# Kernel tuning notes

Measured on AMD Instinct MI355X. Metric: run time of the kernel, lower is better.

## Reference

```python
import jax, jax.numpy as jnp
import numpy as np

B, KOBJ, NS, NK = 32, 100, 16, 8
EMB, FEAT, HID, OUT, COMB = 1024, 2052, 1024, 3000, 512


def _pseudo_coord(bb_centre):
    # bb_centre (B,K,2) -> polar pseudo coords (B,K,K,2) = (rho, theta)
    d = bb_centre[:, :, None, :] - bb_centre[:, None, :, :]
    rho = jnp.sqrt(d[..., 0] ** 2 + d[..., 1] ** 2)
    theta = jnp.arctan2(d[..., 0], d[..., 1])
    return jnp.stack([rho, theta], axis=-1)


def _gauss_weights(pseudo, mr, mt, pr, pt):
    # pseudo (B,K,NS,2); kernel params (NK,) -> weights (B,K,NS,NK)
    rho = pseudo[..., 0:1]
    theta = pseudo[..., 1:2]
    w_rho = jnp.exp(-0.5 * (rho - mr) ** 2 / (1e-14 + pr ** 2))
    fa = jnp.abs(theta - mt)
    sa = jnp.abs(2.0 * jnp.pi - fa)
    w_th = jnp.exp(-0.5 * jnp.minimum(fa, sa) ** 2 / (1e-14 + pt ** 2))
    w = w_rho * w_th
    w = jnp.where(jnp.isnan(w), 0.0, w)
    return w / jnp.sum(w, axis=-1, keepdims=True)  # normalise over kernels


def _graph_conv(feats, pseudo, conv_w, mr, mt, pr, pt):
    # feats (B,K,NS,F), conv_w (NK,F,out_k) -> (B,K,NK*out_k)
    w = _gauss_weights(pseudo, mr, mt, pr, pt)          # (B,K,NS,NK)
    agg = jnp.einsum('bksm,bksf->bkmf', w, feats)       # per-kernel neighbour sum
    out = jnp.einsum('bkmf,mfo->bkmo', agg, conv_w)     # per-kernel linear
    return out.reshape(out.shape[0], out.shape[1], -1)  # kernel-major concat


def _neighbourhood(feats, pseudo, adj, weight):
    # topk over adjacency rows; softmax over topk values (== the per-row loop softmax)
    top_v, top_i = jax.lax.top_k(adj, NS)               # (B,K,NS)
    a = jax.nn.softmax(top_v, axis=-1)
    nb_f = jax.vmap(lambda f, i: f[i])(feats, top_i)    # (B,K,NS,F)
    nb_p = jnp.take_along_axis(pseudo, top_i[..., None], axis=2)  # (B,K,NS,2)
    if weight:
        nb_f = a[..., None] * nb_f
    return nb_f, nb_p


def _forward(question, image, K, W_lproj, b_lproj, W_e1, b_e1, W_e2, b_e2,
             conv_w1, mean_rho1, mean_theta1, prec_rho1, prec_theta1,
             conv_w2, mean_rho2, mean_theta2, prec_rho2, prec_theta2,
             W_o1, b_o1, W_o2, b_o2):
    bb = image[:, :, -4:]
    bb_size = bb[:, :, 2:] - bb[:, :, :2]
    bb_centre = bb[:, :, :2] + 0.5 * bb_size
    pseudo = _pseudo_coord(bb_centre)                   # (B,K,K,2)

    qenc = question @ W_lproj + b_lproj                 # (B,HID)
    qrep = jnp.broadcast_to(qenc[:, None, :], (image.shape[0], K, qenc.shape[-1]))
    cat = jnp.concatenate([image, qrep], axis=-1)       # (B,K,FEAT+HID)

    # GraphLearner: two relu linears then gram matrix
    h = jax.nn.relu(cat @ W_e1 + b_e1)
    h = jax.nn.relu(h @ W_e2 + b_e2)                    # (B,K,COMB)
    adj = jnp.einsum('bkc,blc->bkl', h, h)              # (B,K,K)

    nb_f, nb_p = _neighbourhood(image, pseudo, adj, weight=True)
    g1 = jax.nn.relu(_graph_conv(nb_f, nb_p, conv_w1, mean_rho1, mean_theta1, prec_rho1, prec_theta1))
    nb_f2, nb_p2 = _neighbourhood(g1, pseudo, adj, weight=False)
    g2 = jax.nn.relu(_graph_conv(nb_f2, nb_p2, conv_w2, mean_rho2, mean_theta2, prec_rho2, prec_theta2))
    g2 = jnp.max(g2, axis=1)                            # (B,HID)

    hh = jax.nn.relu(qenc) * g2
    h1 = jax.nn.relu(hh @ W_o1 + b_o1)
    logits = h1 @ W_o2 + b_o2
    return logits, adj


def setup_inputs() -> dict:
    key = jax.random.key(0)
    ks = jax.random.split(key, 17)
    s = jnp.float32(0.02)
    f32 = jnp.float32
    inp = {
        'question': jax.random.normal(ks[0], (B, EMB), f32),
        'image': jax.random.uniform(ks[1], (B, KOBJ, FEAT), f32),
        'K': KOBJ,
        'W_lproj': jax.random.normal(ks[2], (EMB, HID), f32) * s,
        'b_lproj': jnp.zeros((HID,), f32),
        'W_e1': jax.random.normal(ks[3], (FEAT + HID, COMB), f32) * s,
        'b_e1': jnp.zeros((COMB,), f32),
        'W_e2': jax.random.normal(ks[4], (COMB, COMB), f32) * s,
        'b_e2': jnp.zeros((COMB,), f32),
        'conv_w1': jax.random.normal(ks[5], (NK, FEAT, 2 * HID // NK), f32) * s,
        'mean_rho1': jax.random.uniform(ks[6], (NK,), f32),
        'mean_theta1': jax.random.uniform(ks[7], (NK,), f32, -np.pi, np.pi),
        'prec_rho1': jax.random.uniform(ks[8], (NK,), f32),
        'prec_theta1': jax.random.uniform(ks[9], (NK,), f32),
        'conv_w2': jax.random.normal(ks[10], (NK, 2 * HID, HID // NK), f32) * s,
        'mean_rho2': jax.random.uniform(ks[11], (NK,), f32),
        'mean_theta2': jax.random.uniform(ks[12], (NK,), f32, -np.pi, np.pi),
        'prec_rho2': jax.random.uniform(ks[13], (NK,), f32),
        'prec_theta2': jax.random.uniform(ks[14], (NK,), f32),
        'W_o1': jax.random.normal(ks[15], (HID, OUT), f32) * s,
        'b_o1': jnp.zeros((OUT,), f32),
        'W_o2': jax.random.normal(ks[16], (OUT, OUT), f32) * s,
        'b_o2': jnp.zeros((OUT,), f32),
    }
    return inp


def reference(question, image, K, W_lproj, b_lproj, W_e1, b_e1, W_e2, b_e2,
              conv_w1, mean_rho1, mean_theta1, prec_rho1, prec_theta1,
              conv_w2, mean_rho2, mean_theta2, prec_rho2, prec_theta2,
              W_o1, b_o1, W_o2, b_o2):
    return _forward(question, image, K, W_lproj, b_lproj, W_e1, b_e1, W_e2, b_e2,
                    conv_w1, mean_rho1, mean_theta1, prec_rho1, prec_theta1,
                    conv_w2, mean_rho2, mean_theta2, prec_rho2, prec_theta2,
                    W_o1, b_o1, W_o2, b_o2)
```

## Files before the change

### kernel.cpp

```cpp
#include <hip/hip_runtime.h>
#include <math.h>
#include <stdint.h>

#define B_    32
#define KOBJ  100
#define NS_   16
#define NK_   8
#define EMB_  1024
#define FEAT_ 2052
#define HID_  1024
#define OUT_  3000
#define COMB_ 512

#define KP1   2112
#define KP2   2048
#define NO_P  3072
#define KO2   3008

typedef __attribute__((ext_vector_type(8))) short s16x8;
typedef __attribute__((ext_vector_type(4))) float f32x4;

__device__ inline short f2bf(float f) {
  uint32_t u = __builtin_bit_cast(uint32_t, f);
  u = (u + 0x7fff + ((u >> 16) & 1)) >> 16;
  return (short)u;
}
__device__ inline float bf2f(short s) {
  uint32_t u = ((uint32_t)(uint16_t)s) << 16;
  return __builtin_bit_cast(float, u);
}
__device__ inline void gload_lds16(const void* g, void* l) {
  __builtin_amdgcn_global_load_lds(
      (const __attribute__((address_space(1))) void*)g,
      (__attribute__((address_space(3))) void*)l, 16, 0, 0);
}
__device__ inline int xcd_remap(int fid, int nwg) {
  int q = nwg >> 3, r = nwg & 7;
  int x = fid & 7, l = fid >> 3;
  return (x < r ? x * (q + 1) : r * (q + 1) + (x - r) * q) + l;
}

#define IMG_CHUNKS (B_ * KOBJ * (KP1 / 8))
#define IMG_BLKS   ((IMG_CHUNKS + 255) / 256)
#define Q_CHUNKS   (B_ * (EMB_ / 8))
#define Q_BLKS     ((Q_CHUNKS + 255) / 256)
#define C_BLKS     ((B_ * KOBJ + 255) / 256)

__device__ inline void cvt8_split(const float* __restrict__ in, short* __restrict__ oh,
                                  short* __restrict__ ol, int K, int Kp, int idx) {
  int row = idx / (Kp / 8), c8 = (idx % (Kp / 8)) * 8;
  float f[8];
  if (c8 + 8 <= K) {
    const float* src = in + (size_t)row * K + c8;
    float4 a = *(const float4*)src;
    float4 b = *(const float4*)(src + 4);
    f[0] = a.x; f[1] = a.y; f[2] = a.z; f[3] = a.w;
    f[4] = b.x; f[5] = b.y; f[6] = b.z; f[7] = b.w;
  } else {
#pragma unroll
    for (int i = 0; i < 8; ++i) {
      int k = c8 + i;
      f[i] = (k < K) ? in[(size_t)row * K + k] : 0.f;
    }
  }
  s16x8 vh, vl;
#pragma unroll
  for (int i = 0; i < 8; ++i) {
    short h = f2bf(f[i]);
    vh[i] = h;
    vl[i] = f2bf(f[i] - bf2f(h));
  }
  *(s16x8*)(oh + (size_t)row * Kp + c8) = vh;
  *(s16x8*)(ol + (size_t)row * Kp + c8) = vl;
}

struct TD {
  const float* in; short* oh; short* ol;
  int K, N, Kp, OPM, nkt, split, conv, cum;
};
struct TDs { TD d[8]; };

__global__ __launch_bounds__(256) void prep_all(
    TDs ds, int tcum,
    const float* __restrict__ image, const float* __restrict__ question,
    short* __restrict__ imgb, short* __restrict__ imgl,
    short* __restrict__ qh, short* __restrict__ ql, float* __restrict__ cent) {
  int bid = blockIdx.x, t = threadIdx.x;
  if (bid >= tcum) {
    int bb = bid - tcum;
    if (bb < IMG_BLKS) {
      int idx = bb * 256 + t;
      if (idx < IMG_CHUNKS) cvt8_split(image, imgb, imgl, FEAT_, KP1, idx);
    } else if (bb < IMG_BLKS + Q_BLKS) {
      int idx = (bb - IMG_BLKS) * 256 + t;
      if (idx < Q_CHUNKS) cvt8_split(question, qh, ql, EMB_, EMB_, idx);
    } else {
      int i = (bb - IMG_BLKS - Q_BLKS) * 256 + t;
      if (i < B_ * KOBJ) {
        const float* bbx = image + (size_t)i * FEAT_ + (FEAT_ - 4);
        cent[i * 2 + 0] = 0.5f * (bbx[0] + bbx[2]);
        cent[i * 2 + 1] = 0.5f * (bbx[1] + bbx[3]);
      }
    }
    return;
  }
  __shared__ float s[64][65];
  int i = 0;
  while (i < 7 && bid >= ds.d[i].cum) ++i;
  const TD& d = ds.d[i];
  int local = bid - (i ? ds.d[i - 1].cum : 0);
  int k0 = (local % d.nkt) * 64, n0 = (local / d.nkt) * 64;
  int rr = t >> 4, c4 = (t & 15) * 4;
  bool fullN = d.conv || (n0 + 64 <= d.N);
#pragma unroll
  for (int p = 0; p < 4; ++p) {
    int row = p * 16 + rr;
    int kg = k0 + row;
    float v0 = 0.f, v1 = 0.f, v2 = 0.f, v3 = 0.f;
    if (kg < d.K) {
      const float* src = d.conv
          ? d.in + ((size_t)(n0 / d.OPM) * d.K + kg) * d.OPM + (n0 % d.OPM) + c4
          : d.in + (size_t)kg * d.N + n0 + c4;
      if (fullN) {
        float4 v = *(const float4*)src;
        v0 = v.x; v1 = v.y; v2 = v.z; v3 = v.w;
      } else {
        int nb = n0 + c4;
        if (nb + 0 < d.N) v0 = src[0];
        if (nb + 1 < d.N) v1 = src[1];
        if (nb + 2 < d.N) v2 = src[2];
        if (nb + 3 < d.N) v3 = src[3];
      }
    }
    s[row][c4 + 0] = v0; s[row][c4 + 1] = v1;
    s[row][c4 + 2] = v2; s[row][c4 + 3] = v3;
  }
  __syncthreads();
  int nl = t >> 2, kc = (t & 3) << 4;
#pragma unroll
  for (int half = 0; half < 2; ++half) {
    s16x8 vh, vl;
#pragma unroll
    for (int j = 0; j < 8; ++j) {
      float f = s[kc + half * 8 + j][nl];
      short h = f2bf(f);
      vh[j] = h;
      vl[j] = f2bf(f - bf2f(h));
    }
    size_t o = (size_t)(n0 + nl) * d.Kp + k0 + kc + half * 8;
    *(s16x8*)(d.oh + o) = vh;
    if (d.split) *(s16x8*)(d.ol + o) = vl;
  }
}

template <int BM, int BN, int WR, int WC, bool SPLIT, bool RELU, bool BIAS, int OMODE,
          bool SPLITK, bool PB16>
__device__ __forceinline__ void gemm_body(
    char* smem, int bx, int by, int bz,
    const short* __restrict__ Ah, const short* __restrict__ Al,
    const short* __restrict__ Bh, const short* __restrict__ Bl,
    const float* __restrict__ bias,
    float* __restrict__ Cf, short* __restrict__ Ch, short* __restrict__ Cl,
    float* __restrict__ part, short* __restrict__ partb, int KS,
    int M, int N, int Kp, int ldc, int Nw) {
  constexpr int NWV = WR * WC;
  constexpr int WM = BM / WR, WN = BN / WC;
  constexpr int FM = WM / 16, FN = WN / 16;
  constexpr int ACH = BM / 8, BCH = BN / 8;
  constexpr int NCH = (ACH + BCH) * (SPLIT ? 2 : 1);
  char* AshC = smem;
  char* BshC = smem + BM * 128;
  char* AslC = smem + (BM + BN) * 128;
  char* BslC = smem + (2 * BM + BN) * 128;
  int tid = threadIdx.x, wave = tid >> 6, lane = tid & 63;
  int wr = wave / WC, wc = wave % WC;
  int r16 = lane & 15, kq = lane >> 4;
  int m0 = by * BM, n0 = bx * BN;
  int kb = SPLITK ? bz * KS : 0;
  int ke = SPLITK ? (kb + KS < Kp ? kb + KS : Kp) : Kp;
  f32x4 acc[FM][FN] = {};

  for (int k0 = kb; k0 < ke; k0 += 64) {
    __syncthreads();
    for (int c = wave; c < NCH; c += NWV) {
      int cc = c;
      const short* g;
      char* l;
      bool isA;
      if (cc < ACH) { isA = true; g = Ah; l = AshC; }
      else if (SPLIT && cc < 2 * ACH) { cc -= ACH; isA = true; g = Al; l = AslC; }
      else {
        cc -= SPLIT ? 2 * ACH : ACH;
        if (cc < BCH) { isA = false; g = Bh; l = BshC; }
        else { cc -= BCH; isA = false; g = Bl; l = BslC; }
      }
      int Lb = cc * 1024 + lane * 16;
      int row = Lb >> 7;
      int off = (Lb & 127) ^ ((row & 7) << 4);
      const short* gsrc = g + (size_t)((isA ? m0 : n0) + row) * Kp + k0 + (off >> 1);
      gload_lds16(gsrc, l + cc * 1024);
    }
    __syncthreads();
#pragma unroll
    for (int kk = 0; kk < 2; ++kk) {
      int woff = kk * 64 + kq * 16;
      s16x8 ah[FM], al[FM], bh[FN], bl[FN];
#pragma unroll
      for (int f = 0; f < FM; ++f) {
        int row = wr * WM + f * 16 + r16;
        int o = woff ^ ((row & 7) << 4);
        ah[f] = *(const s16x8*)(AshC + row * 128 + o);
        if (SPLIT) al[f] = *(const s16x8*)(AslC + row * 128 + o);
      }
#pragma unroll
      for (int gg = 0; gg < FN; ++gg) {
        int row = wc * WN + gg * 16 + r16;
        int o = woff ^ ((row & 7) << 4);
        bh[gg] = *(const s16x8*)(BshC + row * 128 + o);
        if (SPLIT) bl[gg] = *(const s16x8*)(BslC + row * 128 + o);
      }
#pragma unroll
      for (int f = 0; f < FM; ++f)
#pragma unroll
        for (int gg = 0; gg < FN; ++gg) {
          acc[f][gg] = __builtin_amdgcn_mfma_f32_16x16x32_bf16(ah[f], bh[gg], acc[f][gg], 0, 0, 0);
          if (SPLIT) {
            acc[f][gg] = __builtin_amdgcn_mfma_f32_16x16x32_bf16(ah[f], bl[gg], acc[f][gg], 0, 0, 0);
            acc[f][gg] = __builtin_amdgcn_mfma_f32_16x16x32_bf16(al[f], bh[gg], acc[f][gg], 0, 0, 0);
          }
        }
    }
  }
#pragma unroll
  for (int f = 0; f < FM; ++f)
#pragma unroll
    for (int gg = 0; gg < FN; ++gg)
#pragma unroll
      for (int r = 0; r < 4; ++r) {
        int m = m0 + wr * WM + f * 16 + (lane >> 4) * 4 + r;
        int n = n0 + wc * WN + gg * 16 + r16;
        if (m >= M || n >= Nw) continue;
        float v = (n < N) ? acc[f][gg][r] : 0.f;
        size_t idx = (size_t)m * ldc + n;
        if (SPLITK) {
          size_t pidx = (size_t)bz * M * ldc + idx;
          if (PB16) partb[pidx] = f2bf(v);
          else      part[pidx] = v;
        } else {
          if (BIAS && n < N) v += bias[n];
          if (RELU) v = fmaxf(v, 0.f);
          if (OMODE == 0) Cf[idx] = v;
          else if (OMODE == 1) {
            short h = f2bf(v);
            Ch[idx] = h;
            Cl[idx] = f2bf(v - bf2f(h));
          } else if (OMODE == 2) {
            Ch[idx] = f2bf(v);
          } else {
            Cf[idx] = v;
            short h = f2bf(v);
            Ch[idx] = h;
            Cl[idx] = f2bf(v - bf2f(h));
          }
        }
      }
}

template <int BM, int BN, int WR, int WC, bool SPLIT, bool RELU, bool BIAS, int OMODE,
          bool SPLITK, bool PB16>
__global__ __launch_bounds__(WR * WC * 64) void gemm_mx(
    const short* __restrict__ Ah, const short* __restrict__ Al,
    const short* __restrict__ Bh, const short* __restrict__ Bl,
    const float* __restrict__ bias,
    float* __restrict__ Cf, short* __restrict__ Ch, short* __restrict__ Cl,
    float* __restrict__ part, short* __restrict__ partb, int KS,
    int M, int N, int Kp, int ldc, int Nw) {
  __shared__ char smem_s[(BM + BN) * 128 * (SPLIT ? 2 : 1)];
  int gx = gridDim.x, gy = gridDim.y, gz = gridDim.z;
  int fid = (blockIdx.z * gy + blockIdx.y) * gx + blockIdx.x;
  int wg = xcd_remap(fid, gx * gy * gz);
  int bx = wg % gx, byz = wg / gx;
  int by = byz % gy, bz = byz / gy;
  gemm_body<BM, BN, WR, WC, SPLIT, RELU, BIAS, OMODE, SPLITK, PB16>(
      smem_s, bx, by, bz, Ah, Al, Bh, Bl, bias, Cf, Ch, Cl, part, partb, KS,
      M, N, Kp, ldc, Nw);
}

#define E1B 800
#define P1B 400
__global__ __launch_bounds__(512) void fused_e1_proj1(
    const short* __restrict__ imgb, const short* __restrict__ imgl,
    const short* __restrict__ we1ah, const short* __restrict__ we1al,
    float* __restrict__ partE,
    const short* __restrict__ cw1t, short* __restrict__ proj1b) {
  extern __shared__ char smem[];
  int fid = blockIdx.x;
  if (fid < E1B) {
    int wg = xcd_remap(fid, E1B);
    int gx = COMB_ / 64;
    int bx = wg % gx, t = wg / gx;
    int by = t % (B_ * KOBJ / 128), bz = t / (B_ * KOBJ / 128);
    gemm_body<128, 64, 4, 2, true, false, false, 0, true, false>(
        smem, bx, by, bz, imgb, imgl, we1ah, we1al, nullptr,
        nullptr, nullptr, nullptr, partE, nullptr, 576,
        B_ * KOBJ, COMB_, KP1, COMB_, COMB_);
  } else {
    int wg = xcd_remap(fid - E1B, P1B);
    int gx = 2 * HID_ / 128;
    int bx = wg % gx, by = wg / gx;
    gemm_body<128, 128, 2, 4, false, false, false, 2, false, false>(
        smem, bx, by, 0, imgb, nullptr, cw1t, nullptr, nullptr,
        nullptr, proj1b, nullptr, nullptr, nullptr, 0,
        B_ * KOBJ, 2 * HID_, KP1, 2 * HID_, 2 * HID_);
  }
}

template <int OMODE, bool RELU, bool BIAS, bool BCAST, bool PB16>
__global__ void reduce_split(const float* __restrict__ part, const short* __restrict__ partb,
                             int SK, size_t pstride,
                             const float* __restrict__ bias, const float* __restrict__ bcast,
                             int bcols, float* __restrict__ Cf, short* __restrict__ Ch,
                             short* __restrict__ Cl, int M, int N, int ldIn, int ldOut) {
  int idx4 = blockIdx.x * 256 + threadIdx.x;
  int ld4 = ldIn >> 2;
  if (idx4 >= M * ld4) return;
  int m = idx4 / ld4;
  int n = (idx4 - m * ld4) << 2;
  size_t base = (size_t)m * ldIn + n;
  float a[4] = {0.f, 0.f, 0.f, 0.f};
  for (int s = 0; s < SK; ++s) {
    if (PB16) {
      short4 p = *(const short4*)(partb + (size_t)s * pstride + base);
      const short* pp = (const short*)&p;
#pragma unroll
      for (int j = 0; j < 4; ++j) a[j] += bf2f(pp[j]);
    } else {
      float4 p = *(const float4*)(part + (size_t)s * pstride + base);
      a[0] += p.x; a[1] += p.y; a[2] += p.z; a[3] += p.w;
    }
  }
#pragma unroll
  for (int j = 0; j < 4; ++j) {
    int nn = n + j;
    if (nn < N) {
      if (BCAST) a[j] += bcast[(size_t)(m / KOBJ) * bcols + nn];
      if (BIAS) a[j] += bias[nn];
    }
    if (RELU) a[j] = fmaxf(a[j], 0.f);
  }
  if (n >= ldOut) return;
  size_t o = (size_t)m * ldOut + n;
  if (OMODE == 0) {
    *(float4*)(Cf + o) = make_float4(a[0], a[1], a[2], a[3]);
  } else if (OMODE == 1) {
    short4 hh, ll;
    short* hp = (short*)&hh; short* lp = (short*)&ll;
#pragma unroll
    for (int j = 0; j < 4; ++j) {
      short h = f2bf(a[j]);
      hp[j] = h;
      lp[j] = f2bf(a[j] - bf2f(h));
    }
    *(short4*)(Ch + o) = hh;
    *(short4*)(Cl + o) = ll;
  } else {
    short4 hh;
    short* hp = (short*)&hh;
#pragma unroll
    for (int j = 0; j < 4; ++j) hp[j] = f2bf(a[j]);
    *(short4*)(Ch + o) = hh;
  }
}

__global__ __launch_bounds__(512) void adj_mfma(const short* __restrict__ Hh,
                                                const short* __restrict__ Hl,
                                                float* __restrict__ adj) {
  __shared__ short Ash[128 * 64];
  __shared__ short Asl[128 * 64];
  int tid = threadIdx.x, wave = tid >> 6, lane = tid & 63;
  int wr = wave >> 2, wc = wave & 3;
  int r16 = lane & 15, kq = lane >> 4;
  int b = blockIdx.x;
  const short* baseh = Hh + (size_t)b * KOBJ * COMB_;
  const short* basel = Hl + (size_t)b * KOBJ * COMB_;
  f32x4 acc[4][2] = {};
  for (int k0 = 0; k0 < COMB_; k0 += 64) {
    __syncthreads();
    for (int c = wave; c < 32; c += 8) {
      int cc = c & 15;
      bool hi = c < 16;
      int Lb = cc * 1024 + lane * 16;
      int row = Lb >> 7;
      int off = (Lb & 127) ^ ((row & 7) << 4);
      const short* gsrc = (hi ? baseh : basel) + (size_t)row * COMB_ + k0 + (off >> 1);
      gload_lds16(gsrc, (char*)(hi ? Ash : Asl) + cc * 1024);
    }
    __syncthreads();
#pragma unroll
    for (int kk = 0; kk < 2; ++kk) {
      int woff = kk * 64 + kq * 16;
      s16x8 ah[4], al[4], bh[2], bl[2];
#pragma unroll
      for (int f = 0; f < 4; ++f) {
        int row = wr * 64 + f * 16 + r16;
        int o = woff ^ ((row & 7) << 4);
        ah[f] = *(const s16x8*)((const char*)Ash + row * 128 + o);
        al[f] = *(const s16x8*)((const char*)Asl + row * 128 + o);
      }
#pragma unroll
      for (int g = 0; g < 2; ++g) {
        int row = wc * 32 + g * 16 + r16;
        int o = woff ^ ((row & 7) << 4);
        bh[g] = *(const s16x8*)((const char*)Ash + row * 128 + o);
        bl[g] = *(const s16x8*)((const char*)Asl + row * 128 + o);
      }
#pragma unroll
      for (int f = 0; f < 4; ++f)
#pragma unroll
        for (int g = 0; g < 2; ++g) {
          acc[f][g] = __builtin_amdgcn_mfma_f32_16x16x32_bf16(ah[f], bh[g], acc[f][g], 0, 0, 0);
          acc[f][g] = __builtin_amdgcn_mfma_f32_16x16x32_bf16(ah[f], bl[g], acc[f][g], 0, 0, 0);
          acc[f][g] = __builtin_amdgcn_mfma_f32_16x16x32_bf16(al[f], bh[g], acc[f][g], 0, 0, 0);
        }
    }
  }
#pragma unroll
  for (int f = 0; f < 4; ++f)
#pragma unroll
    for (int g = 0; g < 2; ++g)
#pragma unroll
      for (int r = 0; r < 4; ++r) {
        int m = wr * 64 + f * 16 + (lane >> 4) * 4 + r;
        int n = wc * 32 + g * 16 + r16;
        if (m < KOBJ && n < KOBJ)
          adj[((size_t)b * KOBJ + m) * KOBJ + n] = acc[f][g][r];
      }
}

__global__ __launch_bounds__(256) void topk_weights_kernel(
    const float* __restrict__ adj, const float* __restrict__ cent,
    const float* __restrict__ mr1, const float* __restrict__ mt1,
    const float* __restrict__ pr1, const float* __restrict__ pt1,
    const float* __restrict__ mr2, const float* __restrict__ mt2,
    const float* __restrict__ pr2, const float* __restrict__ pt2,
    int* __restrict__ topi, float* __restrict__ c1, float* __restrict__ c2) {
  int row = blockIdx.x * 4 + (threadIdx.x >> 6);
  int lane = threadIdx.x & 63;
  int b = row / KOBJ, k = row % KOBJ;
  const float* ar = adj + (size_t)row * KOBJ;
  float v0 = (lane < KOBJ) ? ar[lane] : -INFINITY;
  float v1 = (lane + 64 < KOBJ) ? ar[lane + 64] : -INFINITY;
  int i0 = lane, i1 = lane + 64;
  float tv[NS_];
  int ti[NS_];
#pragma unroll
  for (int s = 0; s < NS_; ++s) {
    bool p0 = (v0 > v1) || (v0 == v1 && i0 < i1);
    float bv = p0 ? v0 : v1;
    int bi = p0 ? i0 : i1;
#pragma unroll
    for (int off = 32; off > 0; off >>= 1) {
      float ov = __shfl_xor(bv, off);
      int oi = __shfl_xor(bi, off);
      if (ov > bv || (ov == bv && oi < bi)) { bv = ov; bi = oi; }
    }
    tv[s] = bv; ti[s] = bi;
    if (bi == i0) v0 = -INFINITY;
    if (bi == i1) v1 = -INFINITY;
  }
  float mx = tv[0], sum = 0.f, av[NS_];
#pragma unroll
  for (int s = 0; s < NS_; ++s) { av[s] = expf(tv[s] - mx); sum += av[s]; }
  if (lane < NS_) {
    int j = ti[lane];
    topi[(size_t)row * NS_ + lane] = j;
    float cx = cent[(b * KOBJ + k) * 2 + 0], cy = cent[(b * KOBJ + k) * 2 + 1];
    float dx = cx - cent[(b * KOBJ + j) * 2 + 0];
    float dy = cy - cent[(b * KOBJ + j) * 2 + 1];
    float rho = sqrtf(dx * dx + dy * dy);
    float th = atan2f(dx, dy);
    float w1[NK_], w2[NK_], s1 = 0.f, s2 = 0.f;
#pragma unroll
    for (int m = 0; m < NK_; ++m) {
      {
        float pr = pr1[m], pt = pt1[m], dr = rho - mr1[m];
        float wr = expf(-0.5f * dr * dr / (1e-14f + pr * pr));
        float fa = fabsf(th - mt1[m]);
        float sa = fabsf(6.283185307179586f - fa);
        float da = fminf(fa, sa);
        float wt = expf(-0.5f * da * da / (1e-14f + pt * pt));
        float w = wr * wt;
        if (w != w) w = 0.f;
        w1[m] = w; s1 += w;
      }
      {
        float pr = pr2[m], pt = pt2[m], dr = rho - mr2[m];
        float wr = expf(-0.5f * dr * dr / (1e-14f + pr * pr));
        float fa = fabsf(th - mt2[m]);
        float sa = fabsf(6.283185307179586f - fa);
        float da = fminf(fa, sa);
        float wt = expf(-0.5f * da * da / (1e-14f + pt * pt));
        float w = wr * wt;
        if (w != w) w = 0.f;
        w2[m] = w; s2 += w;
      }
    }
    float as = av[lane] / sum;
#pragma unroll
    for (int m = 0; m < NK_; ++m) {
      c1[((size_t)row * NS_ + lane) * NK_ + m] = as * (w1[m] / s1);
      c2[((size_t)row * NS_ + lane) * NK_ + m] = w2[m] / s2;
    }
  }
}

template <int VEC, bool BF16OUT>
__global__ __launch_bounds__(256) void combine_kernel(
    const short* __restrict__ proj, const float* __restrict__ coeff,
    const int* __restrict__ topi, float* __restrict__ outf, short* __restrict__ outb,
    int N, int mshift) {
  int row = xcd_remap(blockIdx.x, gridDim.x);
  int b = row / KOBJ;
  __shared__ int ids[NS_];
  __shared__ float cs[NS_ * NK_];
  int tid = threadIdx.x;
  if (tid < NS_) ids[tid] = topi[(size_t)row * NS_ + tid];
  else if (tid >= 32 && tid < 32 + NS_ * NK_) cs[tid - 32] = coeff[(size_t)row * NS_ * NK_ + (tid - 32)];
  __syncthreads();
  int n = tid * VEC;
  if (n >= N) return;
  int m = n >> mshift;
  float acc[VEC];
#pragma unroll
  for (int j = 0; j < VEC; ++j) acc[j] = 0.f;
#pragma unroll
  for (int s = 0; s < NS_; ++s) {
    float cc = cs[s * NK_ + m];
    const short* p = proj + ((size_t)b * KOBJ + ids[s]) * N + n;
    if (VEC == 8) {
      s16x8 v = *(const s16x8*)p;
#pragma unroll
      for (int j = 0; j < 8; ++j) acc[j] = fmaf(cc, bf2f(v[j]), acc[j]);
    } else {
      short4 v = *(const short4*)p;
      const short* vp = (const short*)&v;
#pragma unroll
      for (int j = 0; j < 4; ++j) acc[j] = fmaf(cc, bf2f(vp[j]), acc[j]);
    }
  }
#pragma unroll
  for (int j = 0; j < VEC; ++j) acc[j] = fmaxf(acc[j], 0.f);
  if (BF16OUT) {
    if (VEC == 8) {
      s16x8 o;
#pragma unroll
      for (int j = 0; j < 8; ++j) o[j] = f2bf(acc[j]);
      *(s16x8*)(outb + (size_t)row * N + n) = o;
    } else {
      short4 o;
      short* op = (short*)&o;
#pragma unroll
      for (int j = 0; j < 4; ++j) op[j] = f2bf(acc[j]);
      *(short4*)(outb + (size_t)row * N + n) = o;
    }
  } else {
    if (VEC == 4) {
      *(float4*)(outf + (size_t)row * N + n) = make_float4(acc[0], acc[1], acc[2], acc[3]);
    } else {
#pragma unroll
      for (int j = 0; j < VEC; ++j) outf[(size_t)row * N + n + j] = acc[j];
    }
  }
}

__global__ void reduce_hh_kernel(const float* __restrict__ g2, const float* __restrict__ qenc,
                                 short* __restrict__ hhb) {
  int i = blockIdx.x * blockDim.x + threadIdx.x;
  if (i >= B_ * HID_) return;
  int b = i >> 10, n = i & (HID_ - 1);
  const float* p = g2 + (size_t)b * KOBJ * HID_ + n;
  float mx = -INFINITY;
  for (int k = 0; k < KOBJ; ++k) mx = fmaxf(mx, p[(size_t)k * HID_]);
  hhb[i] = f2bf(fmaxf(qenc[i], 0.f) * mx);
}

extern "C" void kernel_launch(void* const* d_in, const int* in_sizes, int n_in,
                              void* d_out, int out_size, void* d_ws, size_t ws_size,
                              hipStream_t stream) {
  const float* question = (const float*)d_in[0];
  const float* image    = (const float*)d_in[1];
  const float* W_lproj  = (const float*)d_in[3];
  const float* b_lproj  = (const float*)d_in[4];
  const float* W_e1     = (const float*)d_in[5];
  const float* b_e1     = (const float*)d_in[6];
  const float* W_e2     = (const float*)d_in[7];
  const float* b_e2     = (const float*)d_in[8];
  const float* conv_w1  = (const float*)d_in[9];
  const float* mr1 = (const float*)d_in[10];
  const float* mt1 = (const float*)d_in[11];
  const float* pr1 = (const float*)d_in[12];
  const float* pt1 = (const float*)d_in[13];
  const float* conv_w2  = (const float*)d_in[14];
  const float* mr2 = (const float*)d_in[15];
  const float* mt2 = (const float*)d_in[16];
  const float* pr2 = (const float*)d_in[17];
  const float* pt2 = (const float*)d_in[18];
  const float* W_o1 = (const float*)d_in[19];
  const float* b_o1 = (const float*)d_in[20];
  const float* W_o2 = (const float*)d_in[21];
  const float* b_o2 = (const float*)d_in[22];

  float* out = (float*)d_out;
  float* logits = out;
  float* adj = out + B_ * OUT_;

  char* ws = (char*)d_ws;
  size_t off = 0;
  auto alloc = [&](size_t bytes) { char* p = ws + off; off += (bytes + 255) & ~((size_t)255); return p; };
  float* qenc  = (float*)alloc((size_t)B_ * HID_ * 4);
  short* qh    = (short*)alloc((size_t)B_ * EMB_ * 2);
  short* ql    = (short*)alloc((size_t)B_ * EMB_ * 2);
  short* qeh   = (short*)alloc((size_t)B_ * HID_ * 2);
  short* qel   = (short*)alloc((size_t)B_ * HID_ * 2);
  short* wlph  = (short*)alloc((size_t)EMB_ * HID_ * 2);
  short* wlpl  = (short*)alloc((size_t)EMB_ * HID_ * 2);
  short* we1ah = (short*)alloc((size_t)COMB_ * KP1 * 2);
  short* we1al = (short*)alloc((size_t)COMB_ * KP1 * 2);
  short* we1bh = (short*)alloc((size_t)COMB_ * HID_ * 2);
  short* we1bl = (short*)alloc((size_t)COMB_ * HID_ * 2);
  short* we2h  = (short*)alloc((size_t)COMB_ * COMB_ * 2);
  short* we2l  = (short*)alloc((size_t)COMB_ * COMB_ * 2);
  float* q1    = (float*)alloc((size_t)B_ * COMB_ * 4);
  short* h1h   = (short*)alloc((size_t)B_ * KOBJ * COMB_ * 2);
  short* h1l   = (short*)alloc((size_t)B_ * KOBJ * COMB_ * 2);
  short* h2h   = (short*)alloc((size_t)(B_ * KOBJ + 128) * COMB_ * 2);
  short* h2l   = (short*)alloc((size_t)(B_ * KOBJ + 128) * COMB_ * 2);
  float* cent  = (float*)alloc((size_t)B_ * KOBJ * 2 * 4);
  int*   topi  = (int*)alloc((size_t)B_ * KOBJ * NS_ * 4);
  float* c1    = (float*)alloc((size_t)B_ * KOBJ * NS_ * NK_ * 4);
  float* c2    = (float*)alloc((size_t)B_ * KOBJ * NS_ * NK_ * 4);
  short* imgb  = (short*)alloc((size_t)B_ * KOBJ * KP1 * 2);
  short* imgl  = (short*)alloc((size_t)B_ * KOBJ * KP1 * 2);
  short* cw1t  = (short*)alloc((size_t)(2 * HID_) * KP1 * 2);
  short* cw2t  = (short*)alloc((size_t)HID_ * KP2 * 2);
  short* proj1b = (short*)alloc((size_t)B_ * KOBJ * 2 * HID_ * 2);
  short* g1b   = (short*)alloc((size_t)B_ * KOBJ * KP2 * 2);
  short* proj2b = (short*)alloc((size_t)B_ * KOBJ * HID_ * 2);
  float* g2    = (float*)alloc((size_t)B_ * KOBJ * HID_ * 4);
  short* hhb   = (short*)alloc((size_t)B_ * HID_ * 2);
  short* wo1t  = (short*)alloc((size_t)NO_P * HID_ * 2);
  short* wo2t  = (short*)alloc((size_t)NO_P * KO2 * 2);
  short* h1ob  = (short*)alloc((size_t)B_ * KO2 * 2);
  float* partE = (float*)alloc((size_t)4 * B_ * KOBJ * COMB_ * 4);
  short* partP = (short*)alloc((size_t)4 * B_ * KOBJ * HID_ * 2);
  (void)ws_size; (void)in_sizes; (void)n_in; (void)out_size;

  dim3 blk(256), blk512(512);

  {
    TDs ds;
    int cum = 0;
    auto set = [&](int i, const float* in, short* oh, short* ol, int K, int N, int Kp,
                   int OPM, int nnt, int split, int conv) {
      int nkt = Kp / 64;
      cum += nkt * nnt;
      ds.d[i] = TD{in, oh, ol, K, N, Kp, OPM, nkt, split, conv, cum};
    };
    set(0, W_lproj, wlph, wlpl, EMB_, HID_, EMB_, 0, HID_ / 64, 1, 0);
    set(1, W_e1, we1ah, we1al, FEAT_, COMB_, KP1, 0, COMB_ / 64, 1, 0);
    set(2, W_e1 + (size_t)FEAT_ * COMB_, we1bh, we1bl, HID_, COMB_, HID_, 0, COMB_ / 64, 1, 0);
    set(3, W_e2, we2h, we2l, COMB_, COMB_, COMB_, 0, COMB_ / 64, 1, 0);
    set(4, conv_w1, cw1t, nullptr, FEAT_, 2 * HID_, KP1, 2 * HID_ / NK_, 2 * HID_ / 64, 0, 1);
    set(5, conv_w2, cw2t, nullptr, 2 * HID_, HID_, KP2, HID_ / NK_, HID_ / 64, 0, 1);
    set(6, W_o1, wo1t, nullptr, HID_, OUT_, HID_, 0, NO_P / 64, 0, 0);
    set(7, W_o2, wo2t, nullptr, OUT_, OUT_, KO2, 0, NO_P / 64, 0, 0);
    prep_all<<<dim3(cum + IMG_BLKS + Q_BLKS + C_BLKS), blk, 0, stream>>>(
        ds, cum, image, question, imgb, imgl, qh, ql, cent);
  }

  gemm_mx<32, 64, 2, 2, true, false, true, 3, false, false><<<dim3(HID_ / 64, 1, 1), blk, 0, stream>>>(
      qh, ql, wlph, wlpl, b_lproj, qenc, qeh, qel, nullptr, nullptr, 0, B_, HID_, EMB_, HID_, HID_);
  gemm_mx<32, 64, 2, 2, true, false, false, 0, false, false><<<dim3(COMB_ / 64, 1, 1), blk, 0, stream>>>(
      qeh, qel, we1bh, we1bl, nullptr, q1, nullptr, nullptr, nullptr, nullptr, 0, B_, COMB_, HID_, COMB_, COMB_);
  fused_e1_proj1<<<dim3(E1B + P1B), blk512, 49152, stream>>>(
      imgb, imgl, we1ah, we1al, partE, cw1t, proj1b);
  reduce_split<1, true, true, true, false><<<dim3(B_ * KOBJ * COMB_ / 4 / 256), blk, 0, stream>>>(
      partE, nullptr, 4, (size_t)B_ * KOBJ * COMB_, b_e1, q1, COMB_, nullptr, h1h, h1l,
      B_ * KOBJ, COMB_, COMB_, COMB_);
  gemm_mx<128, 64, 4, 2, true, false, false, 0, true, false><<<dim3(COMB_ / 64, B_ * KOBJ / 128, 4), blk512, 0, stream>>>(
      h1h, h1l, we2h, we2l, nullptr, nullptr, nullptr, nullptr, partE, nullptr, 128,
      B_ * KOBJ, COMB_, COMB_, COMB_, COMB_);
  reduce_split<1, true, true, false, false><<<dim3(B_ * KOBJ * COMB_ / 4 / 256), blk, 0, stream>>>(
      partE, nullptr, 4, (size_t)B_ * KOBJ * COMB_, b_e2, nullptr, 0, nullptr, h2h, h2l,
      B_ * KOBJ, COMB_, COMB_, COMB_);
  adj_mfma<<<dim3(B_), blk512, 0, stream>>>(h2h, h2l, adj);
  topk_weights_kernel<<<dim3(B_ * KOBJ / 4), blk, 0, stream>>>(
      adj, cent, mr1, mt1, pr1, pt1, mr2, mt2, pr2, pt2, topi, c1, c2);
  combine_kernel<8, true><<<dim3(B_ * KOBJ), blk, 0, stream>>>(
      proj1b, c1, topi, nullptr, g1b, 2 * HID_, 8);
  gemm_mx<128, 128, 2, 4, false, false, false, 0, true, true><<<dim3(HID_ / 128, B_ * KOBJ / 128, 4), blk512, 0, stream>>>(
      g1b, nullptr, cw2t, nullptr, nullptr, nullptr, nullptr, nullptr, nullptr, partP, 512,
      B_ * KOBJ, HID_, KP2, HID_, HID_);
  reduce_split<2, false, false, false, true><<<dim3(B_ * KOBJ * HID_ / 4 / 256), blk, 0, stream>>>(
      nullptr, partP, 4, (size_t)B_ * KOBJ * HID_, nullptr, nullptr, 0, nullptr, proj2b, nullptr,
      B_ * KOBJ, HID_, HID_, HID_);
  combine_kernel<4, false><<<dim3(B_ * KOBJ), blk, 0, stream>>>(
      proj2b, c2, topi, g2, nullptr, HID_, 7);
  reduce_hh_kernel<<<dim3((B_ * HID_ + 255) / 256), blk, 0, stream>>>(g2, qenc, hhb);
  gemm_mx<32, 128, 1, 4, false, false, false, 0, true, false><<<dim3(NO_P / 128, 1, 16), blk, 0, stream>>>(
      hhb, nullptr, wo1t, nullptr, nullptr, nullptr, nullptr, nullptr, partE, nullptr, 64,
      B_, OUT_, HID_, KO2, KO2);
  reduce_split<2, true, true, false, false><<<dim3((B_ * KO2 / 4 + 255) / 256), blk, 0, stream>>>(
      partE, nullptr, 16, (size_t)B_ * KO2, b_o1, nullptr, 0, nullptr, h1ob, nullptr,
      B_, OUT_, KO2, KO2);
  gemm_mx<32, 128, 1, 4, false, false, false, 0, true, false><<<dim3(NO_P / 128, 1, 16), blk, 0, stream>>>(
      h1ob, nullptr, wo2t, nullptr, nullptr, nullptr, nullptr, nullptr, partE, nullptr, 192,
      B_, OUT_, KO2, KO2, KO2);
  reduce_split<0, false, true, false, false><<<dim3((B_ * KO2 / 4 + 255) / 256), blk, 0, stream>>>(
      partE, nullptr, 16, (size_t)B_ * KO2, b_o2, nullptr, 0, logits, nullptr, nullptr,
      B_, OUT_, KO2, OUT_);
}
```

Measured before the change: 318.7 us.

## Fuse question projection into head kernel and fold top-k into adjacency kernel

The question-projection GEMM now runs as extra blocks inside the fused e1/proj1 launch. The e1 split-K factor drops from 4 to 2, which halves the partial buffers the reduce reads. The adjacency MFMA kernel stages its result tile in LDS and runs the top-k and Gaussian weight computation itself, replacing a separate kernel and a global round trip. This saves launches and memory traffic. In exchange the e1 stage has fewer, longer blocks, and the top-k work now runs on only 32 blocks.

```diff
diff --git a/kernel.cpp b/kernel.cpp
--- a/kernel.cpp
+++ b/kernel.cpp
@@ -286,13 +286,18 @@
       M, N, Kp, ldc, Nw);
 }
 
-#define E1B 800
+#define E1B 400
 #define P1B 400
-__global__ __launch_bounds__(512) void fused_e1_proj1(
+#define QEB 16
+__global__ __launch_bounds__(512) void fused_head(
     const short* __restrict__ imgb, const short* __restrict__ imgl,
     const short* __restrict__ we1ah, const short* __restrict__ we1al,
     float* __restrict__ partE,
-    const short* __restrict__ cw1t, short* __restrict__ proj1b) {
+    const short* __restrict__ cw1t, short* __restrict__ proj1b,
+    const short* __restrict__ qh, const short* __restrict__ ql,
+    const short* __restrict__ wlph, const short* __restrict__ wlpl,
+    const float* __restrict__ b_lproj, float* __restrict__ qenc,
+    short* __restrict__ qeh, short* __restrict__ qel) {
   extern __shared__ char smem[];
   int fid = blockIdx.x;
   if (fid < E1B) {
@@ -302,9 +307,9 @@
     int by = t % (B_ * KOBJ / 128), bz = t / (B_ * KOBJ / 128);
     gemm_body<128, 64, 4, 2, true, false, false, 0, true, false>(
         smem, bx, by, bz, imgb, imgl, we1ah, we1al, nullptr,
-        nullptr, nullptr, nullptr, partE, nullptr, 576,
+        nullptr, nullptr, nullptr, partE, nullptr, 1088,
         B_ * KOBJ, COMB_, KP1, COMB_, COMB_);
-  } else {
+  } else if (fid < E1B + P1B) {
     int wg = xcd_remap(fid - E1B, P1B);
     int gx = 2 * HID_ / 128;
     int bx = wg % gx, by = wg / gx;
@@ -312,6 +317,12 @@
         smem, bx, by, 0, imgb, nullptr, cw1t, nullptr, nullptr,
         nullptr, proj1b, nullptr, nullptr, nullptr, 0,
         B_ * KOBJ, 2 * HID_, KP1, 2 * HID_, 2 * HID_);
+  } else {
+    int bx = fid - E1B - P1B;
+    gemm_body<32, 64, 2, 4, true, false, true, 3, false, false>(
+        smem, bx, 0, 0, qh, ql, wlph, wlpl, b_lproj,
+        qenc, qeh, qel, nullptr, nullptr, 0,
+        B_, HID_, EMB_, HID_, HID_);
   }
 }
 
@@ -372,11 +383,18 @@
   }
 }
 
-__global__ __launch_bounds__(512) void adj_mfma(const short* __restrict__ Hh,
-                                                const short* __restrict__ Hl,
-                                                float* __restrict__ adj) {
-  __shared__ short Ash[128 * 64];
-  __shared__ short Asl[128 * 64];
+__global__ __launch_bounds__(512) void adj_topk(
+    const short* __restrict__ Hh, const short* __restrict__ Hl,
+    float* __restrict__ adj, const float* __restrict__ cent,
+    const float* __restrict__ mr1, const float* __restrict__ mt1,
+    const float* __restrict__ pr1, const float* __restrict__ pt1,
+    const float* __restrict__ mr2, const float* __restrict__ mt2,
+    const float* __restrict__ pr2, const float* __restrict__ pt2,
+    int* __restrict__ topi, float* __restrict__ c1, float* __restrict__ c2) {
+  __shared__ char smem[KOBJ * 104 * 4];
+  short* Ash = (short*)smem;
+  short* Asl = (short*)(smem + 16384);
+  float* adjl = (float*)smem;
   int tid = threadIdx.x, wave = tid >> 6, lane = tid & 63;
   int wr = wave >> 2, wc = wave & 3;
   int r16 = lane & 15, kq = lane >> 4;
@@ -424,6 +442,7 @@
         }
     }
   }
+  __syncthreads();
 #pragma unroll
   for (int f = 0; f < 4; ++f)
 #pragma unroll
@@ -432,84 +451,79 @@
       for (int r = 0; r < 4; ++r) {
         int m = wr * 64 + f * 16 + (lane >> 4) * 4 + r;
         int n = wc * 32 + g * 16 + r16;
-        if (m < KOBJ && n < KOBJ)
-          adj[((size_t)b * KOBJ + m) * KOBJ + n] = acc[f][g][r];
-      }
-}
-
-__global__ __launch_bounds__(256) void topk_weights_kernel(
-    const float* __restrict__ adj, const float* __restrict__ cent,
-    const float* __restrict__ mr1, const float* __restrict__ mt1,
-    const float* __restrict__ pr1, const float* __restrict__ pt1,
-    const float* __restrict__ mr2, const float* __restrict__ mt2,
-    const float* __restrict__ pr2, const float* __restrict__ pt2,
-    int* __restrict__ topi, float* __restrict__ c1, float* __restrict__ c2) {
-  int row = blockIdx.x * 4 + (threadIdx.x >> 6);
-  int lane = threadIdx.x & 63;
-  int b = row / KOBJ, k = row % KOBJ;
-  const float* ar = adj + (size_t)row * KOBJ;
-  float v0 = (lane < KOBJ) ? ar[lane] : -INFINITY;
-  float v1 = (lane + 64 < KOBJ) ? ar[lane + 64] : -INFINITY;
-  int i0 = lane, i1 = lane + 64;
-  float tv[NS_];
-  int ti[NS_];
-#pragma unroll
-  for (int s = 0; s < NS_; ++s) {
-    bool p0 = (v0 > v1) || (v0 == v1 && i0 < i1);
-    float bv = p0 ? v0 : v1;
-    int bi = p0 ? i0 : i1;
-#pragma unroll
-    for (int off = 32; off > 0; off >>= 1) {
-      float ov = __shfl_xor(bv, off);
-      int oi = __shfl_xor(bi, off);
-      if (ov > bv || (ov == bv && oi < bi)) { bv = ov; bi = oi; }
-    }
-    tv[s] = bv; ti[s] = bi;
-    if (bi == i0) v0 = -INFINITY;
-    if (bi == i1) v1 = -INFINITY;
-  }
-  float mx = tv[0], sum = 0.f, av[NS_];
-#pragma unroll
-  for (int s = 0; s < NS_; ++s) { av[s] = expf(tv[s] - mx); sum += av[s]; }
-  if (lane < NS_) {
-    int j = ti[lane];
-    topi[(size_t)row * NS_ + lane] = j;
-    float cx = cent[(b * KOBJ + k) * 2 + 0], cy = cent[(b * KOBJ + k) * 2 + 1];
-    float dx = cx - cent[(b * KOBJ + j) * 2 + 0];
-    float dy = cy - cent[(b * KOBJ + j) * 2 + 1];
-    float rho = sqrtf(dx * dx + dy * dy);
-    float th = atan2f(dx, dy);
-    float w1[NK_], w2[NK_], s1 = 0.f, s2 = 0.f;
-#pragma unroll
-    for (int m = 0; m < NK_; ++m) {
-      {
-        float pr = pr1[m], pt = pt1[m], dr = rho - mr1[m];
-        float wr = expf(-0.5f * dr * dr / (1e-14f + pr * pr));
-        float fa = fabsf(th - mt1[m]);
-        float sa = fabsf(6.283185307179586f - fa);
-        float da = fminf(fa, sa);
-        float wt = expf(-0.5f * da * da / (1e-14f + pt * pt));
-        float w = wr * wt;
-        if (w != w) w = 0.f;
-        w1[m] = w; s1 += w;
-      }
-      {
-        float pr = pr2[m], pt = pt2[m], dr = rho - mr2[m];
-        float wr = expf(-0.5f * dr * dr / (1e-14f + pr * pr));
-        float fa = fabsf(th - mt2[m]);
-        float sa = fabsf(6.283185307179586f - fa);
-        float da = fminf(fa, sa);
-        float wt = expf(-0.5f * da * da / (1e-14f + pt * pt));
-        float w = wr * wt;
-        if (w != w) w = 0.f;
-        w2[m] = w; s2 += w;
-      }
-    }
-    float as = av[lane] / sum;
-#pragma unroll
-    for (int m = 0; m < NK_; ++m) {
-      c1[((size_t)row * NS_ + lane) * NK_ + m] = as * (w1[m] / s1);
-      c2[((size_t)row * NS_ + lane) * NK_ + m] = w2[m] / s2;
+        if (m < KOBJ && n < KOBJ) {
+          float v = acc[f][g][r];
+          adjl[m * 104 + n] = v;
+          adj[((size_t)b * KOBJ + m) * KOBJ + n] = v;
+        }
+      }
+  __syncthreads();
+  for (int k = wave; k < KOBJ; k += 8) {
+    const float* ar = adjl + k * 104;
+    float v0 = (lane < KOBJ) ? ar[lane] : -INFINITY;
+    float v1 = (lane + 64 < KOBJ) ? ar[lane + 64] : -INFINITY;
+    int i0 = lane, i1 = lane + 64;
+    float tv[NS_];
+    int ti[NS_];
+#pragma unroll
+    for (int s = 0; s < NS_; ++s) {
+      bool p0 = (v0 > v1) || (v0 == v1 && i0 < i1);
+      float bv = p0 ? v0 : v1;
+      int bi = p0 ? i0 : i1;
+#pragma unroll
+      for (int off = 32; off > 0; off >>= 1) {
+        float ov = __shfl_xor(bv, off);
+        int oi = __shfl_xor(bi, off);
+        if (ov > bv || (ov == bv && oi < bi)) { bv = ov; bi = oi; }
+      }
+      tv[s] = bv; ti[s] = bi;
+      if (bi == i0) v0 = -INFINITY;
+      if (bi == i1) v1 = -INFINITY;
+    }
+    float mx = tv[0], sum = 0.f, av[NS_];
+#pragma unroll
+    for (int s = 0; s < NS_; ++s) { av[s] = expf(tv[s] - mx); sum += av[s]; }
+    if (lane < NS_) {
+      int row = b * KOBJ + k;
+      int j = ti[lane];
+      topi[(size_t)row * NS_ + lane] = j;
+      float cx = cent[row * 2 + 0], cy = cent[row * 2 + 1];
+      float dx = cx - cent[(b * KOBJ + j) * 2 + 0];
+      float dy = cy - cent[(b * KOBJ + j) * 2 + 1];
+      float rho = sqrtf(dx * dx + dy * dy);
+      float th = atan2f(dx, dy);
+      float w1[NK_], w2[NK_], s1 = 0.f, s2 = 0.f;
+#pragma unroll
+      for (int m = 0; m < NK_; ++m) {
+        {
+          float pr = pr1[m], pt = pt1[m], dr = rho - mr1[m];
+          float wr2 = expf(-0.5f * dr * dr / (1e-14f + pr * pr));
+          float fa = fabsf(th - mt1[m]);
+          float sa = fabsf(6.283185307179586f - fa);
+          float da = fminf(fa, sa);
+          float wt = expf(-0.5f * da * da / (1e-14f + pt * pt));
+          float w = wr2 * wt;
+          if (w != w) w = 0.f;
+          w1[m] = w; s1 += w;
+        }
+        {
+          float pr = pr2[m], pt = pt2[m], dr = rho - mr2[m];
+          float wr2 = expf(-0.5f * dr * dr / (1e-14f + pr * pr));
+          float fa = fabsf(th - mt2[m]);
+          float sa = fabsf(6.283185307179586f - fa);
+          float da = fminf(fa, sa);
+          float wt = expf(-0.5f * da * da / (1e-14f + pt * pt));
+          float w = wr2 * wt;
+          if (w != w) w = 0.f;
+          w2[m] = w; s2 += w;
+        }
+      }
+      float as = av[lane] / sum;
+#pragma unroll
+      for (int m = 0; m < NK_; ++m) {
+        c1[((size_t)row * NS_ + lane) * NK_ + m] = as * (w1[m] / s1);
+        c2[((size_t)row * NS_ + lane) * NK_ + m] = w2[m] / s2;
+      }
     }
   }
 }
@@ -678,14 +692,13 @@
         ds, cum, image, question, imgb, imgl, qh, ql, cent);
   }
 
-  gemm_mx<32, 64, 2, 2, true, false, true, 3, false, false><<<dim3(HID_ / 64, 1, 1), blk, 0, stream>>>(
-      qh, ql, wlph, wlpl, b_lproj, qenc, qeh, qel, nullptr, nullptr, 0, B_, HID_, EMB_, HID_, HID_);
+  fused_head<<<dim3(E1B + P1B + QEB), blk512, 49152, stream>>>(
+      imgb, imgl, we1ah, we1al, partE, cw1t, proj1b,
+      qh, ql, wlph, wlpl, b_lproj, qenc, qeh, qel);
   gemm_mx<32, 64, 2, 2, true, false, false, 0, false, false><<<dim3(COMB_ / 64, 1, 1), blk, 0, stream>>>(
       qeh, qel, we1bh, we1bl, nullptr, q1, nullptr, nullptr, nullptr, nullptr, 0, B_, COMB_, HID_, COMB_, COMB_);
-  fused_e1_proj1<<<dim3(E1B + P1B), blk512, 49152, stream>>>(
-      imgb, imgl, we1ah, we1al, partE, cw1t, proj1b);
   reduce_split<1, true, true, true, false><<<dim3(B_ * KOBJ * COMB_ / 4 / 256), blk, 0, stream>>>(
-      partE, nullptr, 4, (size_t)B_ * KOBJ * COMB_, b_e1, q1, COMB_, nullptr, h1h, h1l,
+      partE, nullptr, 2, (size_t)B_ * KOBJ * COMB_, b_e1, q1, COMB_, nullptr, h1h, h1l,
       B_ * KOBJ, COMB_, COMB_, COMB_);
   gemm_mx<128, 64, 4, 2, true, false, false, 0, true, false><<<dim3(COMB_ / 64, B_ * KOBJ / 128, 4), blk512, 0, stream>>>(
       h1h, h1l, we2h, we2l, nullptr, nullptr, nullptr, nullptr, partE, nullptr, 128,
@@ -693,9 +706,8 @@
   reduce_split<1, true, true, false, false><<<dim3(B_ * KOBJ * COMB_ / 4 / 256), blk, 0, stream>>>(
       partE, nullptr, 4, (size_t)B_ * KOBJ * COMB_, b_e2, nullptr, 0, nullptr, h2h, h2l,
       B_ * KOBJ, COMB_, COMB_, COMB_);
-  adj_mfma<<<dim3(B_), blk512, 0, stream>>>(h2h, h2l, adj);
-  topk_weights_kernel<<<dim3(B_ * KOBJ / 4), blk, 0, stream>>>(
-      adj, cent, mr1, mt1, pr1, pt1, mr2, mt2, pr2, pt2, topi, c1, c2);
+  adj_topk<<<dim3(B_), blk512, 0, stream>>>(
+      h2h, h2l, adj, cent, mr1, mt1, pr1, pt1, mr2, mt2, pr2, pt2, topi, c1, c2);
   combine_kernel<8, true><<<dim3(B_ * KOBJ), blk, 0, stream>>>(
       proj1b, c1, topi, nullptr, g1b, 2 * HID_, 8);
   gemm_mx<128, 128, 2, 4, false, false, false, 0, true, true><<<dim3(HID_ / 128, B_ * KOBJ / 128, 4), blk512, 0, stream>>>(
```

Result: slower. 427.1 us (+34.0%).

## Fold question projection into prep kernel and q1 GEMM into head kernel

Applied to the files above, without the earlier changes.

Computes the question projection (question @ W_lproj + b_lproj) directly in fp32 inside the prep kernel, which removes the bf16 split-conversion of W_lproj and question and the separate small GEMM launch. The q1 GEMM (qenc @ W_e1 lower half) becomes extra blocks inside the fused e1/proj1 kernel, removing another launch. Together this cuts two kernel launches and the associated weight conversion traffic. The trade-offs are that the fp32 projection is a scalar FMA loop that each thread runs over all 1024 k values, and the q1 blocks now run with 512-thread blocks and a different warp layout.

```diff
diff --git a/kernel.cpp b/kernel.cpp
--- a/kernel.cpp
+++ b/kernel.cpp
@@ -42,9 +42,8 @@
 
 #define IMG_CHUNKS (B_ * KOBJ * (KP1 / 8))
 #define IMG_BLKS   ((IMG_CHUNKS + 255) / 256)
-#define Q_CHUNKS   (B_ * (EMB_ / 8))
-#define Q_BLKS     ((Q_CHUNKS + 255) / 256)
 #define C_BLKS     ((B_ * KOBJ + 255) / 256)
+#define QE_BLKS    128
 
 __device__ inline void cvt8_split(const float* __restrict__ in, short* __restrict__ oh,
                                   short* __restrict__ ol, int K, int Kp, int idx) {
@@ -78,35 +77,53 @@
   const float* in; short* oh; short* ol;
   int K, N, Kp, OPM, nkt, split, conv, cum;
 };
-struct TDs { TD d[8]; };
+struct TDs { TD d[7]; };
 
 __global__ __launch_bounds__(256) void prep_all(
     TDs ds, int tcum,
     const float* __restrict__ image, const float* __restrict__ question,
-    short* __restrict__ imgb, short* __restrict__ imgl,
-    short* __restrict__ qh, short* __restrict__ ql, float* __restrict__ cent) {
+    short* __restrict__ imgb, short* __restrict__ imgl, float* __restrict__ cent,
+    const float* __restrict__ W_lproj, const float* __restrict__ b_lproj,
+    float* __restrict__ qenc, short* __restrict__ qeh, short* __restrict__ qel) {
+  __shared__ float s[64][65];
+  __shared__ float qrow[EMB_];
   int bid = blockIdx.x, t = threadIdx.x;
   if (bid >= tcum) {
     int bb = bid - tcum;
     if (bb < IMG_BLKS) {
       int idx = bb * 256 + t;
       if (idx < IMG_CHUNKS) cvt8_split(image, imgb, imgl, FEAT_, KP1, idx);
-    } else if (bb < IMG_BLKS + Q_BLKS) {
-      int idx = (bb - IMG_BLKS) * 256 + t;
-      if (idx < Q_CHUNKS) cvt8_split(question, qh, ql, EMB_, EMB_, idx);
-    } else {
-      int i = (bb - IMG_BLKS - Q_BLKS) * 256 + t;
+    } else if (bb < IMG_BLKS + C_BLKS) {
+      int i = (bb - IMG_BLKS) * 256 + t;
       if (i < B_ * KOBJ) {
         const float* bbx = image + (size_t)i * FEAT_ + (FEAT_ - 4);
         cent[i * 2 + 0] = 0.5f * (bbx[0] + bbx[2]);
         cent[i * 2 + 1] = 0.5f * (bbx[1] + bbx[3]);
       }
+    } else {
+      int g = bb - IMG_BLKS - C_BLKS;
+      int b = g >> 2, n0 = (g & 3) << 8;
+      for (int k = t; k < EMB_; k += 256) qrow[k] = question[(size_t)b * EMB_ + k];
+      __syncthreads();
+      int n = n0 + t;
+      float a0 = 0.f, a1 = 0.f, a2 = 0.f, a3 = 0.f;
+      for (int k = 0; k < EMB_; k += 4) {
+        a0 = fmaf(qrow[k + 0], W_lproj[(size_t)(k + 0) * HID_ + n], a0);
+        a1 = fmaf(qrow[k + 1], W_lproj[(size_t)(k + 1) * HID_ + n], a1);
+        a2 = fmaf(qrow[k + 2], W_lproj[(size_t)(k + 2) * HID_ + n], a2);
+        a3 = fmaf(qrow[k + 3], W_lproj[(size_t)(k + 3) * HID_ + n], a3);
+      }
+      float v = (a0 + a1) + (a2 + a3) + b_lproj[n];
+      size_t o = (size_t)b * HID_ + n;
+      qenc[o] = v;
+      short h = f2bf(v);
+      qeh[o] = h;
+      qel[o] = f2bf(v - bf2f(h));
     }
     return;
   }
-  __shared__ float s[64][65];
   int i = 0;
-  while (i < 7 && bid >= ds.d[i].cum) ++i;
+  while (i < 6 && bid >= ds.d[i].cum) ++i;
   const TD& d = ds.d[i];
   int local = bid - (i ? ds.d[i - 1].cum : 0);
   int k0 = (local % d.nkt) * 64, n0 = (local / d.nkt) * 64;
@@ -288,11 +305,15 @@
 
 #define E1B 800
 #define P1B 400
-__global__ __launch_bounds__(512) void fused_e1_proj1(
+#define Q1B 8
+__global__ __launch_bounds__(512) void fused_head(
     const short* __restrict__ imgb, const short* __restrict__ imgl,
     const short* __restrict__ we1ah, const short* __restrict__ we1al,
     float* __restrict__ partE,
-    const short* __restrict__ cw1t, short* __restrict__ proj1b) {
+    const short* __restrict__ cw1t, short* __restrict__ proj1b,
+    const short* __restrict__ qeh, const short* __restrict__ qel,
+    const short* __restrict__ we1bh, const short* __restrict__ we1bl,
+    float* __restrict__ q1) {
   extern __shared__ char smem[];
   int fid = blockIdx.x;
   if (fid < E1B) {
@@ -304,7 +325,7 @@
         smem, bx, by, bz, imgb, imgl, we1ah, we1al, nullptr,
         nullptr, nullptr, nullptr, partE, nullptr, 576,
         B_ * KOBJ, COMB_, KP1, COMB_, COMB_);
-  } else {
+  } else if (fid < E1B + P1B) {
     int wg = xcd_remap(fid - E1B, P1B);
     int gx = 2 * HID_ / 128;
     int bx = wg % gx, by = wg / gx;
@@ -312,6 +333,12 @@
         smem, bx, by, 0, imgb, nullptr, cw1t, nullptr, nullptr,
         nullptr, proj1b, nullptr, nullptr, nullptr, 0,
         B_ * KOBJ, 2 * HID_, KP1, 2 * HID_, 2 * HID_);
+  } else {
+    int bx = fid - E1B - P1B;
+    gemm_body<32, 64, 2, 4, true, false, false, 0, false, false>(
+        smem, bx, 0, 0, qeh, qel, we1bh, we1bl, nullptr,
+        q1, nullptr, nullptr, nullptr, nullptr, 0,
+        B_, COMB_, HID_, COMB_, COMB_);
   }
 }
 
@@ -618,12 +645,8 @@
   size_t off = 0;
   auto alloc = [&](size_t bytes) { char* p = ws + off; off += (bytes + 255) & ~((size_t)255); return p; };
   float* qenc  = (float*)alloc((size_t)B_ * HID_ * 4);
-  short* qh    = (short*)alloc((size_t)B_ * EMB_ * 2);
-  short* ql    = (short*)alloc((size_t)B_ * EMB_ * 2);
   short* qeh   = (short*)alloc((size_t)B_ * HID_ * 2);
   short* qel   = (short*)alloc((size_t)B_ * HID_ * 2);
-  short* wlph  = (short*)alloc((size_t)EMB_ * HID_ * 2);
-  short* wlpl  = (short*)alloc((size_t)EMB_ * HID_ * 2);
   short* we1ah = (short*)alloc((size_t)COMB_ * KP1 * 2);
   short* we1al = (short*)alloc((size_t)COMB_ * KP1 * 2);
   short* we1bh = (short*)alloc((size_t)COMB_ * HID_ * 2);
@@ -666,24 +689,21 @@
       cum += nkt * nnt;
       ds.d[i] = TD{in, oh, ol, K, N, Kp, OPM, nkt, split, conv, cum};
     };
-    set(0, W_lproj, wlph, wlpl, EMB_, HID_, EMB_, 0, HID_ / 64, 1, 0);
-    set(1, W_e1, we1ah, we1al, FEAT_, COMB_, KP1, 0, COMB_ / 64, 1, 0);
-    set(2, W_e1 + (size_t)FEAT_ * COMB_, we1bh, we1bl, HID_, COMB_, HID_, 0, COMB_ / 64, 1, 0);
-    set(3, W_e2, we2h, we2l, COMB_, COMB_, COMB_, 0, COMB_ / 64, 1, 0);
-    set(4, conv_w1, cw1t, nullptr, FEAT_, 2 * HID_, KP1, 2 * HID_ / NK_, 2 * HID_ / 64, 0, 1);
-    set(5, conv_w2, cw2t, nullptr, 2 * HID_, HID_, KP2, HID_ / NK_, HID_ / 64, 0, 1);
-    set(6, W_o1, wo1t, nullptr, HID_, OUT_, HID_, 0, NO_P / 64, 0, 0);
-    set(7, W_o2, wo2t, nullptr, OUT_, OUT_, KO2, 0, NO_P / 64, 0, 0);
-    prep_all<<<dim3(cum + IMG_BLKS + Q_BLKS + C_BLKS), blk, 0, stream>>>(
-        ds, cum, image, question, imgb, imgl, qh, ql, cent);
-  }
-
-  gemm_mx<32, 64, 2, 2, true, false, true, 3, false, false><<<dim3(HID_ / 64, 1, 1), blk, 0, stream>>>(
-      qh, ql, wlph, wlpl, b_lproj, qenc, qeh, qel, nullptr, nullptr, 0, B_, HID_, EMB_, HID_, HID_);
-  gemm_mx<32, 64, 2, 2, true, false, false, 0, false, false><<<dim3(COMB_ / 64, 1, 1), blk, 0, stream>>>(
-      qeh, qel, we1bh, we1bl, nullptr, q1, nullptr, nullptr, nullptr, nullptr, 0, B_, COMB_, HID_, COMB_, COMB_);
-  fused_e1_proj1<<<dim3(E1B + P1B), blk512, 49152, stream>>>(
-      imgb, imgl, we1ah, we1al, partE, cw1t, proj1b);
+    set(0, W_e1, we1ah, we1al, FEAT_, COMB_, KP1, 0, COMB_ / 64, 1, 0);
+    set(1, W_e1 + (size_t)FEAT_ * COMB_, we1bh, we1bl, HID_, COMB_, HID_, 0, COMB_ / 64, 1, 0);
+    set(2, W_e2, we2h, we2l, COMB_, COMB_, COMB_, 0, COMB_ / 64, 1, 0);
+    set(3, conv_w1, cw1t, nullptr, FEAT_, 2 * HID_, KP1, 2 * HID_ / NK_, 2 * HID_ / 64, 0, 1);
+    set(4, conv_w2, cw2t, nullptr, 2 * HID_, HID_, KP2, HID_ / NK_, HID_ / 64, 0, 1);
+    set(5, W_o1, wo1t, nullptr, HID_, OUT_, HID_, 0, NO_P / 64, 0, 0);
+    set(6, W_o2, wo2t, nullptr, OUT_, OUT_, KO2, 0, NO_P / 64, 0, 0);
+    prep_all<<<dim3(cum + IMG_BLKS + C_BLKS + QE_BLKS), blk, 0, stream>>>(
+        ds, cum, image, question, imgb, imgl, cent,
+        W_lproj, b_lproj, qenc, qeh, qel);
+  }
+
+  fused_head<<<dim3(E1B + P1B + Q1B), blk512, 49152, stream>>>(
+      imgb, imgl, we1ah, we1al, partE, cw1t, proj1b,
+      qeh, qel, we1bh, we1bl, q1);
   reduce_split<1, true, true, true, false><<<dim3(B_ * KOBJ * COMB_ / 4 / 256), blk, 0, stream>>>(
       partE, nullptr, 4, (size_t)B_ * KOBJ * COMB_, b_e1, q1, COMB_, nullptr, h1h, h1l,
       B_ * KOBJ, COMB_, COMB_, COMB_);
```

Result: faster. 308.8 us (-3.1%).
